# Optimization experiments

Measured on AMD Instinct MI355X. Metric: run time of the kernel, lower is better.

The kernel has to match this reference:

```python
import jax, jax.numpy as jnp
import numpy as np

NEG_SLOPE = 0.2  # DGL GATConv default leaky_relu slope


def gat_conv(x_src, x_dst, u, v, W, al, ar, b, n_dst):
    """One DGL GATConv: project, SDDMM attention logits, edge softmax over dst, weighted scatter-sum.
    x_src: [Ns, Fin], W: [Fin, H*D], al/ar: [H, D], b: [H*D]. Returns [n_dst, H, D]."""
    H, D = al.shape
    fs = (x_src @ W).reshape(-1, H, D)            # [Ns, H, D]
    fd = (x_dst @ W).reshape(-1, H, D)            # [Nd, H, D]
    el = jnp.sum(fs * al, axis=-1)                # [Ns, H]
    er = jnp.sum(fd * ar, axis=-1)                # [Nd, H]
    e = jax.nn.leaky_relu(el[u] + er[v], NEG_SLOPE)  # [E, H]
    m = jax.ops.segment_max(e, v, num_segments=n_dst)
    m = jnp.where(jnp.isfinite(m), m, 0.0)        # guard empty segments
    ex = jnp.exp(e - m[v])                        # [E, H]
    s = jax.ops.segment_sum(ex, v, num_segments=n_dst)
    a = ex / s[v]                                 # edge softmax weights [E, H]
    out = jax.ops.segment_sum(a[:, :, None] * fs[u], v, num_segments=n_dst)  # [Nd, H, D]
    return out + b.reshape(H, D)


def setup_inputs() -> dict:
    key = jax.random.key(0)
    ks = jax.random.split(key, 16)
    N, E, Fin, H, Dg, Do = 20000, 320000, 256, 8, 32, 32
    sc_in, sc_g = 1.0 / np.sqrt(Fin), 1.0 / np.sqrt(Dg)
    inp = {
        "xA": jax.random.normal(ks[0], (N, Fin), jnp.float32),
        "xB": jax.random.normal(ks[1], (N, Fin), jnp.float32),
        "W1": jax.random.normal(ks[2], (3, Fin, H * Dg), jnp.float32) * sc_in,
        "al1": jax.random.normal(ks[3], (3, H, Dg), jnp.float32) * sc_g,
        "ar1": jax.random.normal(ks[4], (3, H, Dg), jnp.float32) * sc_g,
        "b1": jax.random.normal(ks[5], (3, H * Dg), jnp.float32) * 0.01,
        "W2": jax.random.normal(ks[6], (3, Dg, H * Do), jnp.float32) * sc_g,
        "al2": jax.random.normal(ks[7], (3, H, Do), jnp.float32) * sc_g,
        "ar2": jax.random.normal(ks[8], (3, H, Do), jnp.float32) * sc_g,
        "b2": jax.random.normal(ks[9], (3, H * Do), jnp.float32) * 0.01,
        "u0": jax.random.randint(ks[10], (E,), 0, N, jnp.int32),
        "v0": jax.random.randint(ks[11], (E,), 0, N, jnp.int32),
        "u1": jax.random.randint(ks[12], (E,), 0, N, jnp.int32),
        "v1": jax.random.randint(ks[13], (E,), 0, N, jnp.int32),
        "u2": jax.random.randint(ks[14], (E,), 0, N, jnp.int32),
        "v2": jax.random.randint(ks[15], (E,), 0, N, jnp.int32),
    }
    return inp


def reference(xA, xB, W1, al1, ar1, b1, W2, al2, ar2, b2, u0, v0, u1, v1, u2, v2):
    nA, nB = xA.shape[0], xB.shape[0]
    # layer 1 (i2h): etype0 A->B, etype1 B->A, etype2 A->A; HeteroGraphConv sum over dst type
    hB = gat_conv(xA, xB, u0, v0, W1[0], al1[0], ar1[0], b1[0], nB)
    hA = (gat_conv(xB, xA, u1, v1, W1[1], al1[1], ar1[1], b1[1], nA)
          + gat_conv(xA, xA, u2, v2, W1[2], al1[2], ar1[2], b1[2], nA))
    # mean over heads, then Dropout(eval=identity) + ReLU
    hA = jax.nn.relu(hA.mean(axis=1))
    hB = jax.nn.relu(hB.mean(axis=1))
    # layer 2 (h2o)
    oB = gat_conv(hA, hB, u0, v0, W2[0], al2[0], ar2[0], b2[0], nB)
    oA = (gat_conv(hB, hA, u1, v1, W2[1], al2[1], ar2[1], b2[1], nA)
          + gat_conv(hA, hA, u2, v2, W2[2], al2[2], ar2[2], b2[2], nA))
    # stack {A, B} outputs: [2, N, out_features]
    return jnp.stack([oA.mean(axis=1), oB.mean(axis=1)])
```

## Files before the change

kernel.cpp:

```cpp
#include <hip/hip_runtime.h>
#include <float.h>

#define NEG_SLOPE 0.2f

constexpr int N_NODES = 20000;
constexpr int NE      = 320000;
constexpr int H       = 8;
constexpr int D       = 32;
constexpr int HD      = 256;
constexpr int FIN     = 256;
constexpr int FSZi    = N_NODES * HD;
constexpr int CAP     = 96;
constexpr int NBKT    = 80;
constexpr int BKT_CAP = 5120;

typedef __attribute__((ext_vector_type(8))) short bf16x8;
typedef __attribute__((ext_vector_type(4))) float f32x4;

__device__ __forceinline__ unsigned short f2bf(float x) {
    unsigned u = __float_as_uint(x);
    unsigned r = 0x7FFFu + ((u >> 16) & 1u);
    return (unsigned short)((u + r) >> 16);
}
__device__ __forceinline__ float bf2f(unsigned short h) {
    return __uint_as_float(((unsigned)h) << 16);
}

__device__ __forceinline__ void wlr_calc(const float* W, const float* al,
                                         const float* ar, float* wlr,
                                         int K, int wstride, int t)
{
    int half = t / (3 * K * H);
    int rem  = t % (3 * K * H);
    int et = rem / (K * H);
    int rem2 = rem % (K * H);
    int k = rem2 / H, h = rem2 % H;
    const float* av = (half ? ar : al) + et * HD + h * D;
    const float* Wp = W + (size_t)et * wstride + k * HD + h * D;
    float s = 0.f;
#pragma unroll
    for (int d = 0; d < D; d++) s += Wp[d] * av[d];
    wlr[t] = s;
}

__global__ __launch_bounds__(256) void prep(
    const float* __restrict__ xA, const float* __restrict__ xB,
    const float* __restrict__ W1, const float* __restrict__ al1,
    const float* __restrict__ ar1, const float* __restrict__ b1,
    const float* __restrict__ W2, const float* __restrict__ al2,
    const float* __restrict__ ar2, const float* __restrict__ b2,
    unsigned short* __restrict__ xAb, unsigned short* __restrict__ xBb,
    unsigned short* __restrict__ W1bT, float* __restrict__ bs,
    float* __restrict__ wlr, float* __restrict__ wlr2, int* __restrict__ cur)
{
    const int bid = blockIdx.x;
    const int tid = threadIdx.x;
    if (bid < 10000) {
        int t = bid * 1024 + tid * 4;
        const float* in; unsigned short* outp; int o;
        if (t < FSZi) { in = xA; outp = xAb; o = t; }
        else          { in = xB; outp = xBb; o = t - FSZi; }
        float4 v = *(const float4*)(in + o);
        ushort4 ob;
        ob.x = f2bf(v.x); ob.y = f2bf(v.y); ob.z = f2bf(v.z); ob.w = f2bf(v.w);
        *(ushort4*)(outp + o) = ob;
    } else if (bid < 10192) {
        int idx = (bid - 10000) * 256 + tid;
        int z = idx / 16384, rem = idx % 16384;
        int n = rem / 64, k4 = rem % 64;
        const float* Wz = W1 + (size_t)z * 65536;
        ushort4 ob;
        ob.x = f2bf(Wz[(k4 * 4 + 0) * 256 + n]);
        ob.y = f2bf(Wz[(k4 * 4 + 1) * 256 + n]);
        ob.z = f2bf(Wz[(k4 * 4 + 2) * 256 + n]);
        ob.w = f2bf(Wz[(k4 * 4 + 3) * 256 + n]);
        *(ushort4*)(W1bT + (size_t)z * 65536 + n * 256 + k4 * 4) = ob;
    } else if (bid == 10192) {
        if (tid < 128) {
            int which = tid >> 5, d = tid & 31;
            const float* b = (which < 2) ? b1 : b2;
            float s = 0.f;
            if (which & 1) {
#pragma unroll
                for (int h = 0; h < H; h++) s += b[0 * 256 + h * D + d];
            } else {
#pragma unroll
                for (int h = 0; h < H; h++) s += b[1 * 256 + h * D + d] + b[2 * 256 + h * D + d];
            }
            bs[tid] = s;
        }
    } else if (bid < 10241) {
        int t = (bid - 10193) * 256 + tid;
        wlr_calc(W1, al1, ar1, wlr, 256, 65536, t);
    } else if (bid < 10247) {
        int t = (bid - 10241) * 256 + tid;
        wlr_calc(W2, al2, ar2, wlr2, 32, 8192, t);
    } else {
        if (tid < 3 * NBKT) cur[tid] = 0;
    }
}

__global__ __launch_bounds__(256) void bucket_a(
    const int* __restrict__ u0, const int* __restrict__ v0,
    const int* __restrict__ u1, const int* __restrict__ v1,
    const int* __restrict__ u2, const int* __restrict__ v2,
    int* __restrict__ cur, unsigned* __restrict__ bucketed)
{
    const int et = blockIdx.y;
    const int* up = (et == 0) ? u0 : (et == 1) ? u1 : u2;
    const int* vp = (et == 0) ? v0 : (et == 1) ? v1 : v2;
    const int CHUNK = NE / 32;
    const int e0 = blockIdx.x * CHUNK;
    __shared__ int hist[NBKT], base[NBKT], lcur[NBKT];
    if (threadIdx.x < NBKT) hist[threadIdx.x] = 0;
    __syncthreads();
    for (int i = e0 + threadIdx.x; i < e0 + CHUNK; i += 256)
        atomicAdd(&hist[vp[i] >> 8], 1);
    __syncthreads();
    if (threadIdx.x < NBKT) {
        base[threadIdx.x] = atomicAdd(&cur[et * NBKT + threadIdx.x], hist[threadIdx.x]);
        lcur[threadIdx.x] = 0;
    }
    __syncthreads();
    for (int i = e0 + threadIdx.x; i < e0 + CHUNK; i += 256) {
        int v = vp[i], u = up[i];
        int bkt = v >> 8;
        int pos = base[bkt] + atomicAdd(&lcur[bkt], 1);
        bucketed[(size_t)(et * NBKT + bkt) * BKT_CAP + pos] =
            ((unsigned)v << 16) | (unsigned)u;
    }
}

__global__ __launch_bounds__(256) void bucket_b(
    const int* __restrict__ cur, const unsigned* __restrict__ bucketed,
    int* __restrict__ cnt, int* __restrict__ usort)
{
    const int et = blockIdx.y, bkt = blockIdx.x;
    const int nbase = bkt << 8;
    __shared__ int cl[256];
    cl[threadIdx.x] = 0;
    __syncthreads();
    const int count = cur[et * NBKT + bkt];
    const unsigned* src = bucketed + (size_t)(et * NBKT + bkt) * BKT_CAP;
    for (int i = threadIdx.x; i < count; i += 256) {
        unsigned e = src[i];
        int v = (int)(e >> 16), u = (int)(e & 0xFFFFu);
        int slot = atomicAdd(&cl[v - nbase], 1);
        usort[(size_t)(et * N_NODES + v) * CAP + slot] = u;
    }
    __syncthreads();
    int node = nbase + threadIdx.x;
    if (node < N_NODES) cnt[et * N_NODES + node] = cl[threadIdx.x];
}

__global__ __launch_bounds__(256) void mfma_gemm3(
    const unsigned short* __restrict__ xAb, const unsigned short* __restrict__ xBb,
    const unsigned short* __restrict__ W1bT, unsigned short* __restrict__ Fb, int M)
{
    const int z = blockIdx.z;
    const unsigned short* Xb = (z == 1) ? xBb : xAb;
    const unsigned short* WzT = W1bT + (size_t)z * 65536;
    unsigned short* F = Fb + (size_t)z * FSZi;

    __shared__ unsigned short Xs[2][128][40];
    const int tid = threadIdx.x;
    const int wid = tid >> 6, lane = tid & 63;
    const int r0 = blockIdx.x * 128;
    const int c0 = blockIdx.y * 64;
    const int l15 = lane & 15, lg = lane >> 4;

    f32x4 acc[2][4];
#pragma unroll
    for (int i = 0; i < 2; i++)
#pragma unroll
        for (int j = 0; j < 4; j++) acc[i][j] = (f32x4){0.f, 0.f, 0.f, 0.f};

    const int srow = tid >> 2, sq = tid & 3;
    bf16x8 bcur[4], bnxt[4];

    {
        int grow0 = r0 + srow, grow1 = r0 + srow + 64;
        *(int4*)&Xs[0][srow][sq * 8] =
            (grow0 < M) ? *(const int4*)(Xb + (size_t)grow0 * FIN + sq * 8) : make_int4(0,0,0,0);
        *(int4*)&Xs[0][srow + 64][sq * 8] =
            (grow1 < M) ? *(const int4*)(Xb + (size_t)grow1 * FIN + sq * 8) : make_int4(0,0,0,0);
    }
#pragma unroll
    for (int j = 0; j < 4; j++)
        bcur[j] = *(const bf16x8*)(WzT + (size_t)(c0 + j * 16 + l15) * 256 + lg * 8);
    __syncthreads();

    for (int s = 0; s < 8; s++) {
        int cur2 = s & 1, nb = cur2 ^ 1;
        if (s < 7) {
            int kc = (s + 1) * 32;
            int grow0 = r0 + srow, grow1 = r0 + srow + 64;
            *(int4*)&Xs[nb][srow][sq * 8] =
                (grow0 < M) ? *(const int4*)(Xb + (size_t)grow0 * FIN + kc + sq * 8) : make_int4(0,0,0,0);
            *(int4*)&Xs[nb][srow + 64][sq * 8] =
                (grow1 < M) ? *(const int4*)(Xb + (size_t)grow1 * FIN + kc + sq * 8) : make_int4(0,0,0,0);
#pragma unroll
            for (int j = 0; j < 4; j++)
                bnxt[j] = *(const bf16x8*)(WzT + (size_t)(c0 + j * 16 + l15) * 256 + kc + lg * 8);
        }
        const int rm = wid * 32;
        bf16x8 a0 = *(const bf16x8*)&Xs[cur2][rm + l15][lg * 8];
        bf16x8 a1 = *(const bf16x8*)&Xs[cur2][rm + 16 + l15][lg * 8];
#pragma unroll
        for (int j = 0; j < 4; j++) {
            acc[0][j] = __builtin_amdgcn_mfma_f32_16x16x32_bf16(a0, bcur[j], acc[0][j], 0, 0, 0);
            acc[1][j] = __builtin_amdgcn_mfma_f32_16x16x32_bf16(a1, bcur[j], acc[1][j], 0, 0, 0);
        }
        __syncthreads();
#pragma unroll
        for (int j = 0; j < 4; j++) bcur[j] = bnxt[j];
    }
    const int rm = wid * 32;
#pragma unroll
    for (int i = 0; i < 2; i++)
#pragma unroll
        for (int j = 0; j < 4; j++)
#pragma unroll
            for (int r = 0; r < 4; r++) {
                int row = r0 + rm + i * 16 + lg * 4 + r;
                if (row < M)
                    F[(size_t)row * 256 + c0 + j * 16 + l15] = f2bf(acc[i][j][r]);
            }
}

__global__ __launch_bounds__(256) void gemm32_3(
    const float* __restrict__ hA, const float* __restrict__ hB,
    const float* __restrict__ W2, unsigned short* __restrict__ Fb, int M)
{
    const int z = blockIdx.z;
    const float* X = (z == 1) ? hB : hA;
    const float* W = W2 + (size_t)z * 8192;
    unsigned short* F = Fb + (size_t)z * FSZi;

    __shared__ float Xs[128][40];
    __shared__ float Ws[32][64];
    const int tx = threadIdx.x & 15;
    const int ty = threadIdx.x >> 4;
    const int r0 = blockIdx.x * 128;
    const int c0 = blockIdx.y * 64;
    for (int idx = threadIdx.x; idx < 128 * 8; idx += 256) {
        int row = idx >> 3, kq = idx & 7;
        int grow = r0 + row;
        float4 xv = (grow < M) ? *(const float4*)(X + (size_t)grow * 32 + kq * 4)
                               : make_float4(0.f, 0.f, 0.f, 0.f);
        *(float4*)&Xs[row][kq * 4] = xv;
    }
    for (int idx = threadIdx.x; idx < 32 * 16; idx += 256) {
        int k = idx >> 4, cq = idx & 15;
        *(float4*)&Ws[k][cq * 4] = *(const float4*)(W + (size_t)k * 256 + c0 + cq * 4);
    }
    __syncthreads();
    float4 acc[8];
#pragma unroll
    for (int r = 0; r < 8; r++) acc[r] = make_float4(0.f, 0.f, 0.f, 0.f);
#pragma unroll 4
    for (int k = 0; k < 32; k++) {
        float4 wv = *(float4*)&Ws[k][tx * 4];
#pragma unroll
        for (int r = 0; r < 8; r++) {
            float x = Xs[ty + 16 * r][k];
            acc[r].x = fmaf(x, wv.x, acc[r].x);
            acc[r].y = fmaf(x, wv.y, acc[r].y);
            acc[r].z = fmaf(x, wv.z, acc[r].z);
            acc[r].w = fmaf(x, wv.w, acc[r].w);
        }
    }
#pragma unroll
    for (int r = 0; r < 8; r++) {
        int row = r0 + ty + 16 * r;
        if (row < M) {
            ushort4 cb;
            cb.x = f2bf(acc[r].x); cb.y = f2bf(acc[r].y);
            cb.z = f2bf(acc[r].z); cb.w = f2bf(acc[r].w);
            *(ushort4*)(F + (size_t)row * 256 + c0 + tx * 4) = cb;
        }
    }
}

template <int K>
__global__ __launch_bounds__(256) void gemv6(
    const float* __restrict__ xa, const float* __restrict__ xb,
    const float* __restrict__ wlr,
    float* __restrict__ el, float* __restrict__ er, int N)
{
    __shared__ float w[4][K * H];
    const int KH = K * H;
    const int NH = N_NODES * H;
    float *o0, *o1, *o2, *o3;
    const float* x;
    if (blockIdx.y == 0) {
        for (int i = threadIdx.x; i < KH; i += 256) {
            w[0][i] = wlr[0 * KH + i];
            w[1][i] = wlr[4 * KH + i];
            w[2][i] = wlr[2 * KH + i];
            w[3][i] = wlr[5 * KH + i];
        }
        x = xa;
        o0 = el; o1 = er + NH; o2 = el + 2 * NH; o3 = er + 2 * NH;
    } else {
        for (int i = threadIdx.x; i < KH; i += 256) {
            w[0][i] = wlr[1 * KH + i];
            w[1][i] = wlr[3 * KH + i];
        }
        x = xb;
        o0 = el + NH; o1 = er; o2 = nullptr; o3 = nullptr;
    }
    __syncthreads();
    int t = blockIdx.x * 256 + threadIdx.x;
    if (t >= N * H) return;
    int n = t >> 3, h = t & 7;
    const float4* xp = (const float4*)(x + (size_t)n * K);
    float s0 = 0.f, s1 = 0.f, s2 = 0.f, s3 = 0.f;
    if (blockIdx.y == 0) {
#pragma unroll 2
        for (int k4 = 0; k4 < K / 4; k4++) {
            float4 xv = xp[k4];
            const float* xe = &xv.x;
#pragma unroll
            for (int e = 0; e < 4; e++) {
                int idx = (4 * k4 + e) * H + h;
                float xx = xe[e];
                s0 = fmaf(xx, w[0][idx], s0);
                s1 = fmaf(xx, w[1][idx], s1);
                s2 = fmaf(xx, w[2][idx], s2);
                s3 = fmaf(xx, w[3][idx], s3);
            }
        }
        o0[t] = s0; o1[t] = s1; o2[t] = s2; o3[t] = s3;
    } else {
#pragma unroll 2
        for (int k4 = 0; k4 < K / 4; k4++) {
            float4 xv = xp[k4];
            const float* xe = &xv.x;
#pragma unroll
            for (int e = 0; e < 4; e++) {
                int idx = (4 * k4 + e) * H + h;
                float xx = xe[e];
                s0 = fmaf(xx, w[0][idx], s0);
                s1 = fmaf(xx, w[1][idx], s1);
            }
        }
        o0[t] = s0; o1[t] = s1;
    }
}


__device__ __forceinline__ float lrelu(float e) {
    return (e >= 0.f) ? e : NEG_SLOPE * e;
}

__device__ __forceinline__ float4 seg_accum(
    const float* __restrict__ el, float erh,
    const int* __restrict__ us, int lo, int hi,
    const unsigned short* __restrict__ Fs, int lane, int h)
{
    float4 aa = make_float4(0.f, 0.f, 0.f, 0.f);
    if (lo >= hi) return aa;
    const int q = lane & 7;
    const int lbase = lane & 56;
    float s = 0.f;
    int j = lo;
    for (; j + 8 <= hi; j += 8) {
        int u[8];
#pragma unroll
        for (int qq = 0; qq < 8; qq++) u[qq] = us[j + qq];
        ushort4 fb[8];
#pragma unroll
        for (int qq = 0; qq < 8; qq++)
            fb[qq] = *(const ushort4*)(Fs + ((size_t)u[qq] << 8) + lane * 4);
        float myw = __expf(lrelu(el[u[q] * H + h] + erh));
#pragma unroll
        for (int qq = 0; qq < 8; qq++) {
            float w = __shfl(myw, lbase + qq, 64);
            s += w;
            aa.x = fmaf(w, bf2f(fb[qq].x), aa.x);
            aa.y = fmaf(w, bf2f(fb[qq].y), aa.y);
            aa.z = fmaf(w, bf2f(fb[qq].z), aa.z);
            aa.w = fmaf(w, bf2f(fb[qq].w), aa.w);
        }
    }
    if (j < hi) {
        int rem = hi - j;
        int u[8];
#pragma unroll
        for (int qq = 0; qq < 8; qq++) u[qq] = us[(qq < rem) ? j + qq : hi - 1];
        ushort4 fb[8];
#pragma unroll
        for (int qq = 0; qq < 8; qq++)
            fb[qq] = *(const ushort4*)(Fs + ((size_t)u[qq] << 8) + lane * 4);
        float myw = (q < rem) ? __expf(lrelu(el[u[q] * H + h] + erh)) : 0.f;
#pragma unroll
        for (int qq = 0; qq < 8; qq++) {
            float w = __shfl(myw, lbase + qq, 64);
            s += w;
            aa.x = fmaf(w, bf2f(fb[qq].x), aa.x);
            aa.y = fmaf(w, bf2f(fb[qq].y), aa.y);
            aa.z = fmaf(w, bf2f(fb[qq].z), aa.z);
            aa.w = fmaf(w, bf2f(fb[qq].w), aa.w);
        }
    }
    float inv = (s > 0.f) ? 1.f / s : 0.f;
    aa.x *= inv; aa.y *= inv; aa.z *= inv; aa.w *= inv;
    return aa;
}

template <int RELU>
__global__ __launch_bounds__(256) void seg_att_all(
    const float* __restrict__ el0, const float* __restrict__ er0,
    const unsigned short* __restrict__ F0,
    const float* __restrict__ el1, const float* __restrict__ er1,
    const unsigned short* __restrict__ F1,
    const float* __restrict__ el2, const float* __restrict__ er2,
    const unsigned short* __restrict__ F2,
    const int* __restrict__ cnt, const int* __restrict__ us,
    const float* __restrict__ bsB, const float* __restrict__ bsA,
    float* __restrict__ outB, float* __restrict__ outA, int N)
{
    int wid = blockIdx.x * 4 + (threadIdx.x >> 6);
    if (wid >= 2 * N) return;
    const int lane = threadIdx.x & 63;
    const int h = lane >> 3;
    float4 tot;
    const float* bs;
    float* out;
    int v;
    if (wid < N) {
        v = wid;
        int lo = v * CAP;
        tot = seg_accum(el0, er0[v * H + h], us, lo, lo + cnt[v], F0, lane, h);
        bs = bsB; out = outB;
    } else {
        v = wid - N;
        int lo1 = (N_NODES + v) * CAP;
        int lo2 = (2 * N_NODES + v) * CAP;
        float4 t1 = seg_accum(el1, er1[v * H + h], us, lo1, lo1 + cnt[N_NODES + v], F1, lane, h);
        float4 t2 = seg_accum(el2, er2[v * H + h], us, lo2, lo2 + cnt[2 * N_NODES + v], F2, lane, h);
        tot.x = t1.x + t2.x; tot.y = t1.y + t2.y;
        tot.z = t1.z + t2.z; tot.w = t1.w + t2.w;
        bs = bsA; out = outA;
    }
#pragma unroll
    for (int mask = 8; mask <= 32; mask <<= 1) {
        tot.x += __shfl_xor(tot.x, mask, 64);
        tot.y += __shfl_xor(tot.y, mask, 64);
        tot.z += __shfl_xor(tot.z, mask, 64);
        tot.w += __shfl_xor(tot.w, mask, 64);
    }
    if (lane < 8) {
        float4 b = *(const float4*)(bs + lane * 4);
        float4 o;
        o.x = (tot.x + b.x) * 0.125f;
        o.y = (tot.y + b.y) * 0.125f;
        o.z = (tot.z + b.z) * 0.125f;
        o.w = (tot.w + b.w) * 0.125f;
        if (RELU) {
            o.x = fmaxf(o.x, 0.f); o.y = fmaxf(o.y, 0.f);
            o.z = fmaxf(o.z, 0.f); o.w = fmaxf(o.w, 0.f);
        }
        *(float4*)(out + (size_t)v * D + lane * 4) = o;
    }
}


extern "C" void kernel_launch(void* const* d_in, const int* in_sizes, int n_in,
                              void* d_out, int out_size, void* d_ws, size_t ws_size,
                              hipStream_t stream)
{
    const float* xA  = (const float*)d_in[0];
    const float* xB  = (const float*)d_in[1];
    const float* W1  = (const float*)d_in[2];
    const float* al1 = (const float*)d_in[3];
    const float* ar1 = (const float*)d_in[4];
    const float* b1  = (const float*)d_in[5];
    const float* W2  = (const float*)d_in[6];
    const float* al2 = (const float*)d_in[7];
    const float* ar2 = (const float*)d_in[8];
    const float* b2  = (const float*)d_in[9];
    const int* u0 = (const int*)d_in[10];
    const int* v0 = (const int*)d_in[11];
    const int* u1 = (const int*)d_in[12];
    const int* v1 = (const int*)d_in[13];
    const int* u2 = (const int*)d_in[14];
    const int* v2 = (const int*)d_in[15];
    float* out = (float*)d_out;

    const size_t FSZ = (size_t)FSZi;
    unsigned short* xAb  = (unsigned short*)d_ws;
    unsigned short* xBb  = xAb + FSZ;
    unsigned short* Fb   = xBb + FSZ;
    unsigned short* F0b  = Fb;
    unsigned short* F1b  = Fb + FSZ;
    unsigned short* F2b  = Fb + 2 * FSZ;
    unsigned short* W1bT = Fb + 3 * FSZ;
    float* el   = (float*)(W1bT + 3 * 65536);
    float* er   = el + 3 * N_NODES * H;
    float* hA   = er + 3 * N_NODES * H;
    float* hB   = hA + (size_t)N_NODES * D;
    float* wlr  = hB + (size_t)N_NODES * D;
    float* wlr2 = wlr + 6 * 2048;
    float* bs   = wlr2 + 6 * 256;
    int* cnt    = (int*)(bs + 128);
    int* cur    = cnt + 3 * N_NODES;
    unsigned* bucketed = (unsigned*)(cur + 3 * NBKT);
    int* usort  = (int*)(bucketed + (size_t)3 * NBKT * BKT_CAP);

    float* el0 = el, *el1p = el + N_NODES * H, *el2p = el + 2 * N_NODES * H;
    float* er0 = er, *er1p = er + N_NODES * H, *er2p = er + 2 * N_NODES * H;
    float* bsA1 = bs, *bsB1 = bs + 32, *bsA2 = bs + 64, *bsB2 = bs + 96;

    const dim3 GB_MM3(157, 4, 3);
    const dim3 GB_GV(N_NODES * H / 256, 2);
    const dim3 GB_BA(32, 3);
    const dim3 GB_BB(NBKT, 3);
    const int GB_ALL = (2 * N_NODES + 3) / 4;
    const int PREP_B = 10248;

    prep<<<PREP_B, 256, 0, stream>>>(xA, xB, W1, al1, ar1, b1, W2, al2, ar2, b2,
                                     xAb, xBb, W1bT, bs, wlr, wlr2, cur);
    bucket_a<<<GB_BA, 256, 0, stream>>>(u0, v0, u1, v1, u2, v2, cur, bucketed);
    bucket_b<<<GB_BB, 256, 0, stream>>>(cur, bucketed, cnt, usort);

    mfma_gemm3<<<GB_MM3, 256, 0, stream>>>(xAb, xBb, W1bT, Fb, N_NODES);
    gemv6<256><<<GB_GV, 256, 0, stream>>>(xA, xB, wlr, el, er, N_NODES);
    seg_att_all<1><<<GB_ALL, 256, 0, stream>>>(el0, er0, F0b,
                                               el1p, er1p, F1b,
                                               el2p, er2p, F2b,
                                               cnt, usort, bsB1, bsA1, hB, hA, N_NODES);

    gemm32_3<<<GB_MM3, 256, 0, stream>>>(hA, hB, W2, Fb, N_NODES);
    gemv6<32><<<GB_GV, 256, 0, stream>>>(hA, hB, wlr2, el, er, N_NODES);
    seg_att_all<0><<<GB_ALL, 256, 0, stream>>>(el0, er0, F0b,
                                               el1p, er1p, F1b,
                                               el2p, er2p, F2b,
                                               cnt, usort, bsB2, bsA2,
                                               out + (size_t)N_NODES * D, out, N_NODES);
}
```

Baseline: 281.8 us.

## Aggregate 32-dim hidden features before projection in layer-two GAT

Layer two no longer projects hA/hB to 256-wide bf16 features and gathers those per edge. It gathers the 32-wide fp32 hidden rows, weighting each head separately, into a per-node [8×32] aggregate. A new epilogue GEMM then applies per-head-reorganised W2 (built in prep), adds bias and averages over heads. This cuts per-edge gather width and removes the layer-two projection kernel. The cost is a large fp32 intermediate (three N×256 buffers reusing the layer-one workspace) that must be written and read back, plus a simple FMA-based epilogue GEMM.

```diff
diff --git a/kernel.cpp b/kernel.cpp
--- a/kernel.cpp
+++ b/kernel.cpp
@@ -51,7 +51,8 @@
     const float* __restrict__ ar2, const float* __restrict__ b2,
     unsigned short* __restrict__ xAb, unsigned short* __restrict__ xBb,
     unsigned short* __restrict__ W1bT, float* __restrict__ bs,
-    float* __restrict__ wlr, float* __restrict__ wlr2, int* __restrict__ cur)
+    float* __restrict__ wlr, float* __restrict__ wlr2,
+    int* __restrict__ cur, float* __restrict__ W2h)
 {
     const int bid = blockIdx.x;
     const int tid = threadIdx.x;
@@ -95,8 +96,14 @@
     } else if (bid < 10247) {
         int t = (bid - 10241) * 256 + tid;
         wlr_calc(W2, al2, ar2, wlr2, 32, 8192, t);
+    } else if (bid == 10247) {
+        if (tid < 3 * NBKT) cur[tid] = 0;
     } else {
-        if (tid < 3 * NBKT) cur[tid] = 0;
+        int idx = (bid - 10248) * 256 + tid;
+        int et = idx / 8192, rem = idx % 8192;
+        int hk = rem / 32, d = rem % 32;
+        int h = hk >> 5, k = hk & 31;
+        W2h[idx] = W2[(size_t)et * 8192 + k * 256 + h * 32 + d];
     }
 }
 
@@ -228,60 +235,6 @@
             }
 }
 
-__global__ __launch_bounds__(256) void gemm32_3(
-    const float* __restrict__ hA, const float* __restrict__ hB,
-    const float* __restrict__ W2, unsigned short* __restrict__ Fb, int M)
-{
-    const int z = blockIdx.z;
-    const float* X = (z == 1) ? hB : hA;
-    const float* W = W2 + (size_t)z * 8192;
-    unsigned short* F = Fb + (size_t)z * FSZi;
-
-    __shared__ float Xs[128][40];
-    __shared__ float Ws[32][64];
-    const int tx = threadIdx.x & 15;
-    const int ty = threadIdx.x >> 4;
-    const int r0 = blockIdx.x * 128;
-    const int c0 = blockIdx.y * 64;
-    for (int idx = threadIdx.x; idx < 128 * 8; idx += 256) {
-        int row = idx >> 3, kq = idx & 7;
-        int grow = r0 + row;
-        float4 xv = (grow < M) ? *(const float4*)(X + (size_t)grow * 32 + kq * 4)
-                               : make_float4(0.f, 0.f, 0.f, 0.f);
-        *(float4*)&Xs[row][kq * 4] = xv;
-    }
-    for (int idx = threadIdx.x; idx < 32 * 16; idx += 256) {
-        int k = idx >> 4, cq = idx & 15;
-        *(float4*)&Ws[k][cq * 4] = *(const float4*)(W + (size_t)k * 256 + c0 + cq * 4);
-    }
-    __syncthreads();
-    float4 acc[8];
-#pragma unroll
-    for (int r = 0; r < 8; r++) acc[r] = make_float4(0.f, 0.f, 0.f, 0.f);
-#pragma unroll 4
-    for (int k = 0; k < 32; k++) {
-        float4 wv = *(float4*)&Ws[k][tx * 4];
-#pragma unroll
-        for (int r = 0; r < 8; r++) {
-            float x = Xs[ty + 16 * r][k];
-            acc[r].x = fmaf(x, wv.x, acc[r].x);
-            acc[r].y = fmaf(x, wv.y, acc[r].y);
-            acc[r].z = fmaf(x, wv.z, acc[r].z);
-            acc[r].w = fmaf(x, wv.w, acc[r].w);
-        }
-    }
-#pragma unroll
-    for (int r = 0; r < 8; r++) {
-        int row = r0 + ty + 16 * r;
-        if (row < M) {
-            ushort4 cb;
-            cb.x = f2bf(acc[r].x); cb.y = f2bf(acc[r].y);
-            cb.z = f2bf(acc[r].z); cb.w = f2bf(acc[r].w);
-            *(ushort4*)(F + (size_t)row * 256 + c0 + tx * 4) = cb;
-        }
-    }
-}
-
 template <int K>
 __global__ __launch_bounds__(256) void gemv6(
     const float* __restrict__ xa, const float* __restrict__ xb,
@@ -348,7 +301,6 @@
         o0[t] = s0; o1[t] = s1;
     }
 }
-
 
 __device__ __forceinline__ float lrelu(float e) {
     return (e >= 0.f) ? e : NEG_SLOPE * e;
@@ -466,6 +418,157 @@
     }
 }
 
+__device__ __forceinline__ float4 seg_accum_h(
+    const float* __restrict__ el, float erh,
+    const int* __restrict__ us, int lo, int hi,
+    const float* __restrict__ htab, int lane, int h)
+{
+    float4 aa = make_float4(0.f, 0.f, 0.f, 0.f);
+    if (lo >= hi) return aa;
+    const int q = lane & 7;
+    const int q4 = q * 4;
+    const int lbase = lane & 56;
+    float s = 0.f;
+    int j = lo;
+    for (; j + 8 <= hi; j += 8) {
+        int u[8];
+#pragma unroll
+        for (int qq = 0; qq < 8; qq++) u[qq] = us[j + qq];
+        float4 fb[8];
+#pragma unroll
+        for (int qq = 0; qq < 8; qq++)
+            fb[qq] = *(const float4*)(htab + (size_t)u[qq] * 32 + q4);
+        float myw = __expf(lrelu(el[u[q] * H + h] + erh));
+#pragma unroll
+        for (int qq = 0; qq < 8; qq++) {
+            float w = __shfl(myw, lbase + qq, 64);
+            s += w;
+            aa.x = fmaf(w, fb[qq].x, aa.x);
+            aa.y = fmaf(w, fb[qq].y, aa.y);
+            aa.z = fmaf(w, fb[qq].z, aa.z);
+            aa.w = fmaf(w, fb[qq].w, aa.w);
+        }
+    }
+    if (j < hi) {
+        int rem = hi - j;
+        int u[8];
+#pragma unroll
+        for (int qq = 0; qq < 8; qq++) u[qq] = us[(qq < rem) ? j + qq : hi - 1];
+        float4 fb[8];
+#pragma unroll
+        for (int qq = 0; qq < 8; qq++)
+            fb[qq] = *(const float4*)(htab + (size_t)u[qq] * 32 + q4);
+        float myw = (q < rem) ? __expf(lrelu(el[u[q] * H + h] + erh)) : 0.f;
+#pragma unroll
+        for (int qq = 0; qq < 8; qq++) {
+            float w = __shfl(myw, lbase + qq, 64);
+            s += w;
+            aa.x = fmaf(w, fb[qq].x, aa.x);
+            aa.y = fmaf(w, fb[qq].y, aa.y);
+            aa.z = fmaf(w, fb[qq].z, aa.z);
+            aa.w = fmaf(w, fb[qq].w, aa.w);
+        }
+    }
+    float inv = (s > 0.f) ? 1.f / s : 0.f;
+    aa.x *= inv; aa.y *= inv; aa.z *= inv; aa.w *= inv;
+    return aa;
+}
+
+__global__ __launch_bounds__(256) void seg_att_l2(
+    const float* __restrict__ el0, const float* __restrict__ er0,
+    const float* __restrict__ el1, const float* __restrict__ er1,
+    const float* __restrict__ el2, const float* __restrict__ er2,
+    const float* __restrict__ hA, const float* __restrict__ hB,
+    const int* __restrict__ cnt, const int* __restrict__ us,
+    float* __restrict__ agg0, float* __restrict__ agg1,
+    float* __restrict__ agg2, int N)
+{
+    int wid = blockIdx.x * 4 + (threadIdx.x >> 6);
+    if (wid >= 2 * N) return;
+    const int lane = threadIdx.x & 63;
+    const int h = lane >> 3;
+    if (wid < N) {
+        int v = wid;
+        int lo = v * CAP;
+        float4 aa = seg_accum_h(el0, er0[v * H + h], us, lo, lo + cnt[v], hA, lane, h);
+        *(float4*)(agg0 + (size_t)v * 256 + lane * 4) = aa;
+    } else {
+        int v = wid - N;
+        int lo1 = (N_NODES + v) * CAP;
+        int lo2 = (2 * N_NODES + v) * CAP;
+        float4 a1 = seg_accum_h(el1, er1[v * H + h], us, lo1, lo1 + cnt[N_NODES + v], hB, lane, h);
+        float4 a2 = seg_accum_h(el2, er2[v * H + h], us, lo2, lo2 + cnt[2 * N_NODES + v], hA, lane, h);
+        *(float4*)(agg1 + (size_t)v * 256 + lane * 4) = a1;
+        *(float4*)(agg2 + (size_t)v * 256 + lane * 4) = a2;
+    }
+}
+
+__global__ __launch_bounds__(256) void ep_gemm(
+    const float* __restrict__ agg0, const float* __restrict__ agg1,
+    const float* __restrict__ agg2, const float* __restrict__ W2h,
+    const float* __restrict__ bsA, const float* __restrict__ bsB,
+    float* __restrict__ outA, float* __restrict__ outB, int N)
+{
+    __shared__ float Xs[128][68];
+    __shared__ float Ws[64][32];
+    const int tid = threadIdx.x;
+    const int tx = tid & 7, ty = tid >> 3;
+    const int r0 = blockIdx.x * 128;
+    const int isA = (blockIdx.y == 0);
+    const int nmat = isA ? 2 : 1;
+
+    float4 acc[4];
+#pragma unroll
+    for (int r = 0; r < 4; r++) acc[r] = make_float4(0.f, 0.f, 0.f, 0.f);
+
+    for (int m = 0; m < nmat; m++) {
+        const float* agg = isA ? (m ? agg2 : agg1) : agg0;
+        const float* w   = W2h + (size_t)(isA ? (m ? 2 : 1) : 0) * 8192;
+        for (int kc = 0; kc < 256; kc += 64) {
+            for (int i = tid; i < 128 * 16; i += 256) {
+                int row = i >> 4, kq = i & 15;
+                int grow = r0 + row;
+                float4 xv = (grow < N) ? *(const float4*)(agg + (size_t)grow * 256 + kc + kq * 4)
+                                       : make_float4(0.f, 0.f, 0.f, 0.f);
+                *(float4*)&Xs[row][kq * 4] = xv;
+            }
+            for (int i = tid; i < 64 * 8; i += 256) {
+                int k = i >> 3, cq = i & 7;
+                *(float4*)&Ws[k][cq * 4] = *(const float4*)(w + (size_t)(kc + k) * 32 + cq * 4);
+            }
+            __syncthreads();
+#pragma unroll 4
+            for (int k = 0; k < 64; k++) {
+                float4 wv = *(float4*)&Ws[k][tx * 4];
+#pragma unroll
+                for (int r = 0; r < 4; r++) {
+                    float x = Xs[ty + 32 * r][k];
+                    acc[r].x = fmaf(x, wv.x, acc[r].x);
+                    acc[r].y = fmaf(x, wv.y, acc[r].y);
+                    acc[r].z = fmaf(x, wv.z, acc[r].z);
+                    acc[r].w = fmaf(x, wv.w, acc[r].w);
+                }
+            }
+            __syncthreads();
+        }
+    }
+    const float* bs = isA ? bsA : bsB;
+    float* out = isA ? outA : outB;
+    float4 b = *(const float4*)(bs + tx * 4);
+#pragma unroll
+    for (int r = 0; r < 4; r++) {
+        int row = r0 + ty + 32 * r;
+        if (row < N) {
+            float4 o;
+            o.x = (acc[r].x + b.x) * 0.125f;
+            o.y = (acc[r].y + b.y) * 0.125f;
+            o.z = (acc[r].z + b.z) * 0.125f;
+            o.w = (acc[r].w + b.w) * 0.125f;
+            *(float4*)(out + (size_t)row * 32 + tx * 4) = o;
+        }
+    }
+}
+
 
 extern "C" void kernel_launch(void* const* d_in, const int* in_sizes, int n_in,
                               void* d_out, int out_size, void* d_ws, size_t ws_size,
@@ -497,13 +600,20 @@
     unsigned short* F1b  = Fb + FSZ;
     unsigned short* F2b  = Fb + 2 * FSZ;
     unsigned short* W1bT = Fb + 3 * FSZ;
-    float* el   = (float*)(W1bT + 3 * 65536);
+
+    float* agg0 = (float*)d_ws;
+    float* agg1 = agg0 + (size_t)N_NODES * 256;
+    float* agg2 = agg1 + (size_t)N_NODES * 256;
+    const size_t AGG_BYTES = (size_t)3 * N_NODES * 256 * 4;
+
+    float* el   = (float*)((char*)d_ws + AGG_BYTES);
     float* er   = el + 3 * N_NODES * H;
     float* hA   = er + 3 * N_NODES * H;
     float* hB   = hA + (size_t)N_NODES * D;
     float* wlr  = hB + (size_t)N_NODES * D;
     float* wlr2 = wlr + 6 * 2048;
-    float* bs   = wlr2 + 6 * 256;
+    float* W2h  = wlr2 + 6 * 256;
+    float* bs   = W2h + 3 * 8192;
     int* cnt    = (int*)(bs + 128);
     int* cur    = cnt + 3 * N_NODES;
     unsigned* bucketed = (unsigned*)(cur + 3 * NBKT);
@@ -517,11 +627,12 @@
     const dim3 GB_GV(N_NODES * H / 256, 2);
     const dim3 GB_BA(32, 3);
     const dim3 GB_BB(NBKT, 3);
+    const dim3 GB_EP(157, 2);
     const int GB_ALL = (2 * N_NODES + 3) / 4;
-    const int PREP_B = 10248;
+    const int PREP_B = 10248 + 96;
 
     prep<<<PREP_B, 256, 0, stream>>>(xA, xB, W1, al1, ar1, b1, W2, al2, ar2, b2,
-                                     xAb, xBb, W1bT, bs, wlr, wlr2, cur);
+                                     xAb, xBb, W1bT, bs, wlr, wlr2, cur, W2h);
     bucket_a<<<GB_BA, 256, 0, stream>>>(u0, v0, u1, v1, u2, v2, cur, bucketed);
     bucket_b<<<GB_BB, 256, 0, stream>>>(cur, bucketed, cnt, usort);
 
@@ -532,11 +643,10 @@
                                                el2p, er2p, F2b,
                                                cnt, usort, bsB1, bsA1, hB, hA, N_NODES);
 
-    gemm32_3<<<GB_MM3, 256, 0, stream>>>(hA, hB, W2, Fb, N_NODES);
     gemv6<32><<<GB_GV, 256, 0, stream>>>(hA, hB, wlr2, el, er, N_NODES);
-    seg_att_all<0><<<GB_ALL, 256, 0, stream>>>(el0, er0, F0b,
-                                               el1p, er1p, F1b,
-                                               el2p, er2p, F2b,
-                                               cnt, usort, bsB2, bsA2,
-                                               out + (size_t)N_NODES * D, out, N_NODES);
-}
+    seg_att_l2<<<GB_ALL, 256, 0, stream>>>(el0, er0, el1p, er1p, el2p, er2p,
+                                           hA, hB, cnt, usort,
+                                           agg0, agg1, agg2, N_NODES);
+    ep_gemm<<<GB_EP, 256, 0, stream>>>(agg0, agg1, agg2, W2h, bsA2, bsB2,
+                                       out, out + (size_t)N_NODES * D, N_NODES);
+}
```

Measured after the change: 298.6 us. +6.0%, slower.
